# Optimization experiments

Hardware: AMD Instinct MI355X
Metric: run time of the kernel (lower is better)

The kernel has to match this reference:

```python
import jax, jax.numpy as jnp
import numpy as np

N = 50000      # nodes
E = 600000     # edges (avg degree 12)
D = 128        # input_dim == hidden_dim (required: same Linear reused across pool layers)
OUT = 64       # output_dim
NUM_POOL = 2   # num_pool_layers


def setup_inputs() -> dict:
    key = jax.random.key(0)
    ks = jax.random.split(key, 8)
    s = 1.0 / np.sqrt(D)  # fan-in style scaling keeps repeated scatter-adds stable
    x = jax.random.normal(ks[0], (N, D), dtype=jnp.float32)
    edge_index = jax.random.randint(ks[1], (2, E), 0, N, dtype=jnp.int64)
    W1 = jax.random.normal(ks[2], (D, D), dtype=jnp.float32) * s
    b1 = jnp.zeros((D,), dtype=jnp.float32)
    W2 = jax.random.normal(ks[3], (D, D), dtype=jnp.float32) * s
    b2 = jnp.zeros((D,), dtype=jnp.float32)
    Wout = jax.random.normal(ks[4], (D, OUT), dtype=jnp.float32) * s
    bout = jnp.zeros((OUT,), dtype=jnp.float32)
    return {"x": x, "edge_index": edge_index, "W1": W1, "b1": b1,
            "W2": W2, "b2": b2, "Wout": Wout, "bout": bout}


def _gauss_seidel_pool(x, W, b, src, dst, num_layers):
    # PyG MessagePassing(aggr='add'): out[i] = sum_{edges (j->i)} lin(x[j]).
    # Nodes with no incoming edges become zero (propagate replaces x entirely).
    for _ in range(num_layers):
        m = x @ W + b                      # [N, out] linear once per node (== lin(x_j) per edge)
        x = jax.ops.segment_sum(m[src], dst, num_segments=N)  # gather + scatter-add
    return x


def reference(x, edge_index, W1, b1, W2, b2, Wout, bout):
    src = edge_index[0]  # x_j source
    dst = edge_index[1]  # aggregation target i
    h = _gauss_seidel_pool(x, W1, b1, src, dst, NUM_POOL)
    h = jax.nn.relu(h)                     # dropout = identity (eval mode)
    h = _gauss_seidel_pool(h, W2, b2, src, dst, NUM_POOL)
    h = jax.nn.relu(h)
    return h @ Wout + bout                 # [N, OUT]
```

## Files before the change

kernel.cpp:

```cpp
#include <hip/hip_runtime.h>


static inline int ceil_div(int a, int b) { return (a + b - 1) / b; }

typedef __attribute__((ext_vector_type(8))) short bf16x8;
typedef __attribute__((ext_vector_type(4))) float f32x4;
typedef __attribute__((ext_vector_type(2))) float f32x2;

__device__ inline unsigned short f2bf(float f) {
    unsigned u = __float_as_uint(f);
    return (unsigned short)((u + 0x7fffu + ((u >> 16) & 1u)) >> 16);
}

__device__ inline unsigned char f2fp8(float f) {
    return (unsigned char)(__builtin_amdgcn_cvt_pk_fp8_f32(f, 0.f, 0u, false) & 0xffu);
}


__device__ void wprep_dev(const float* __restrict__ W, unsigned short* __restrict__ hi,
                          int total, int C, int g0, int G) {
    for (int t = g0; t < total; t += G) {
        int j = t & 7;
        int lane = (t >> 3) & 63;
        int f = t >> 9;
        int c = f & 3, ct = f >> 2;
        int k = c * 32 + (lane >> 4) * 8 + j;
        int col = ct * 16 + (lane & 15);
        hi[t] = f2bf(W[(size_t)k * C + col]);
    }
}

__global__ __launch_bounds__(256) void prep_kernel(const float* __restrict__ x,
                                                   const float* __restrict__ W1,
                                                   const float* __restrict__ W2,
                                                   const float* __restrict__ Wout,
                                                   unsigned char* __restrict__ xb,
                                                   unsigned short* __restrict__ W1hi,
                                                   unsigned short* __restrict__ W2hi,
                                                   unsigned short* __restrict__ Wohi,
                                                   int* __restrict__ cursor,
                                                   unsigned* __restrict__ stat,
                                                   int N, int nChunks) {
    int g0 = blockIdx.x * 256 + threadIdx.x;
    int G = gridDim.x * 256;
    for (int i = g0; i < N; i += G) cursor[i] = 0;
    for (int i = g0; i < nChunks; i += G) stat[i] = 0;

    int nq = N * 32;
    for (int i = g0; i < nq; i += G) {
        float4 v = ((const float4*)x)[i];
        unsigned w = __builtin_amdgcn_cvt_pk_fp8_f32(v.x, v.y, 0u, false);
        w = __builtin_amdgcn_cvt_pk_fp8_f32(v.z, v.w, w, true);
        ((unsigned*)xb)[i] = w;
    }

    wprep_dev(W1, W1hi, 128 * 128, 128, g0, G);
    wprep_dev(W2, W2hi, 128 * 128, 128, g0, G);
    wprep_dev(Wout, Wohi, 128 * 64, 64, g0, G);
}


__global__ __launch_bounds__(256) void hist_kernel(const int* __restrict__ dst,
                                                   int* __restrict__ deg, int E) {
    int e = blockIdx.x * 256 + threadIdx.x;
    if (e < E) atomicAdd(&deg[dst[e]], 1);
}

__global__ __launch_bounds__(256) void scan_fuse_kernel(const int* __restrict__ deg,
                                                        int* __restrict__ rp,
                                                        int* __restrict__ cursor,
                                                        unsigned* __restrict__ stat,
                                                        int N) {
    __shared__ int s[256];
    int c = blockIdx.x, tid = threadIdx.x;
    int i = c * 256 + tid;
    int v = (i < N) ? deg[i] : 0;
    s[tid] = v;
    __syncthreads();
    for (int off = 1; off < 256; off <<= 1) {
        int t = (tid >= off) ? s[tid - off] : 0;
        __syncthreads();
        s[tid] += t;
        __syncthreads();
    }
    int loc = s[tid] - v;
    int tot = s[255];
    __syncthreads();
    if (tid == 0) atomicExch(&stat[c], (unsigned)tot | 0x80000000u);

    unsigned mine = 0;
    if (tid < c) {
        unsigned u;
        do { u = atomicAdd(&stat[tid], 0u); } while (!(u & 0x80000000u));
        mine = u & 0x7fffffffu;
    }
    s[tid] = (int)mine;
    __syncthreads();
    for (int off = 128; off >= 1; off >>= 1) {
        if (tid < off) s[tid] += s[tid + off];
        __syncthreads();
    }
    int prefix = s[0];
    if (i <= N) {
        int val = loc + prefix;
        rp[i] = val;
        if (i < N) cursor[i] = val;
    }
}

__global__ __launch_bounds__(256) void fill_kernel(const int* __restrict__ src,
                                                   const int* __restrict__ dst,
                                                   int* __restrict__ cursor,
                                                   unsigned short* __restrict__ es, int E) {
    int e = blockIdx.x * 256 + threadIdx.x;
    if (e < E) {
        int p = atomicAdd(&cursor[dst[e]], 1);
        es[p] = (unsigned short)src[e];
    }
}


__device__ inline void acc_fp8(float* a, uint2 v) {
    f32x2 p;
    p = __builtin_amdgcn_cvt_pk_f32_fp8(v.x, false); a[0] += p[0]; a[1] += p[1];
    p = __builtin_amdgcn_cvt_pk_f32_fp8(v.x, true);  a[2] += p[0]; a[3] += p[1];
    p = __builtin_amdgcn_cvt_pk_f32_fp8(v.y, false); a[4] += p[0]; a[5] += p[1];
    p = __builtin_amdgcn_cvt_pk_f32_fp8(v.y, true);  a[6] += p[0]; a[7] += p[1];
}

template <bool RELU, bool OUTCHAIN>
__global__ __launch_bounds__(256) void fused_kernel(const unsigned char* __restrict__ M,
                                                    const int* __restrict__ rp,
                                                    const unsigned short* __restrict__ es,
                                                    const uint4* __restrict__ Whi,
                                                    const float* __restrict__ bvec,
                                                    const uint4* __restrict__ Wof,
                                                    const float* __restrict__ bout,
                                                    void* __restrict__ Yv, int n) {
    constexpr int SR = 136;
    constexpr int ECAP = 1280;
    __shared__ unsigned short Hl[64 * SR];
    __shared__ unsigned short esl[ECAP];
    __shared__ int rpl[65];
    __shared__ unsigned char perm[64];

    int tid = threadIdx.x;
    int r0 = blockIdx.x * 64;

    if (tid < 65) {
        int gi = r0 + tid;
        if (gi > n) gi = n;
        rpl[tid] = rp[gi];
    }
    __syncthreads();

    int ebase = rpl[0];
    int ecnt = rpl[64] - ebase;
    if (ecnt > ECAP) ecnt = ECAP;

    if (tid < 64) {
        int di = rpl[tid + 1] - rpl[tid];
        int rank = 0;
        for (int j = 0; j < 64; ++j) {
            int dj = rpl[j + 1] - rpl[j];
            rank += (dj > di) || (dj == di && j < tid);
        }
        perm[rank] = (unsigned char)tid;
    }
    for (int i = tid; i < ecnt; i += 256) esl[i] = es[ebase + i];
    __syncthreads();

    {
        int g = tid >> 4, ln = tid & 15;
        const unsigned char* Mh = M + ln * 8;
#pragma unroll 1
        for (int q = 0; q < 4; ++q) {
            int nl = perm[q * 16 + g];
            int pbeg = rpl[nl] - ebase, pend = rpl[nl + 1] - ebase;
            int pm = pend < ecnt ? pend : ecnt;
            float acc[8] = {};
            int p = pbeg;
            for (; p + 8 <= pm; p += 8) {
                int s0 = esl[p],     s1 = esl[p + 1], s2 = esl[p + 2], s3 = esl[p + 3];
                int s4 = esl[p + 4], s5 = esl[p + 5], s6 = esl[p + 6], s7 = esl[p + 7];
                uint2 v0 = *(const uint2*)(Mh + (size_t)s0 * 128);
                uint2 v1 = *(const uint2*)(Mh + (size_t)s1 * 128);
                uint2 v2 = *(const uint2*)(Mh + (size_t)s2 * 128);
                uint2 v3 = *(const uint2*)(Mh + (size_t)s3 * 128);
                uint2 v4 = *(const uint2*)(Mh + (size_t)s4 * 128);
                uint2 v5 = *(const uint2*)(Mh + (size_t)s5 * 128);
                uint2 v6 = *(const uint2*)(Mh + (size_t)s6 * 128);
                uint2 v7 = *(const uint2*)(Mh + (size_t)s7 * 128);
                acc_fp8(acc, v0); acc_fp8(acc, v1);
                acc_fp8(acc, v2); acc_fp8(acc, v3);
                acc_fp8(acc, v4); acc_fp8(acc, v5);
                acc_fp8(acc, v6); acc_fp8(acc, v7);
            }
            for (; p + 4 <= pm; p += 4) {
                int s0 = esl[p], s1 = esl[p + 1], s2 = esl[p + 2], s3 = esl[p + 3];
                uint2 v0 = *(const uint2*)(Mh + (size_t)s0 * 128);
                uint2 v1 = *(const uint2*)(Mh + (size_t)s1 * 128);
                uint2 v2 = *(const uint2*)(Mh + (size_t)s2 * 128);
                uint2 v3 = *(const uint2*)(Mh + (size_t)s3 * 128);
                acc_fp8(acc, v0); acc_fp8(acc, v1);
                acc_fp8(acc, v2); acc_fp8(acc, v3);
            }
            for (; p < pm; ++p) {
                uint2 v = *(const uint2*)(Mh + (size_t)esl[p] * 128);
                acc_fp8(acc, v);
            }
            for (; p < pend; ++p) {
                uint2 v = *(const uint2*)(Mh + (size_t)es[ebase + p] * 128);
                acc_fp8(acc, v);
            }
            uint4 o;
            o.x = (unsigned)f2bf(acc[0]) | ((unsigned)f2bf(acc[1]) << 16);
            o.y = (unsigned)f2bf(acc[2]) | ((unsigned)f2bf(acc[3]) << 16);
            o.z = (unsigned)f2bf(acc[4]) | ((unsigned)f2bf(acc[5]) << 16);
            o.w = (unsigned)f2bf(acc[6]) | ((unsigned)f2bf(acc[7]) << 16);
            *(uint4*)(&Hl[nl * SR + ln * 8]) = o;
        }
    }
    __syncthreads();

    int wave = tid >> 6, lane = tid & 63;
    int lm = lane & 15, lq = lane >> 4;

    f32x4 acc[4][2];
#pragma unroll
    for (int rt = 0; rt < 4; ++rt)
#pragma unroll
        for (int t = 0; t < 2; ++t)
            acc[rt][t] = (f32x4){0.f, 0.f, 0.f, 0.f};

#pragma unroll
    for (int c = 0; c < 4; ++c) {
        bf16x8 afr[4];
#pragma unroll
        for (int rt = 0; rt < 4; ++rt)
            afr[rt] = *(const bf16x8*)(&Hl[(rt * 16 + lm) * SR + c * 32 + lq * 8]);
#pragma unroll
        for (int t = 0; t < 2; ++t) {
            int ct = wave * 2 + t;
            uint4 uh = Whi[(ct * 4 + c) * 64 + lane];
            bf16x8 wh = *(const bf16x8*)&uh;
#pragma unroll
            for (int rt = 0; rt < 4; ++rt)
                acc[rt][t] = __builtin_amdgcn_mfma_f32_16x16x32_bf16(afr[rt], wh, acc[rt][t], 0, 0, 0);
        }
    }

    if (!OUTCHAIN) {
#pragma unroll
        for (int t = 0; t < 2; ++t) {
            int col = (wave * 2 + t) * 16 + lm;
            float bv = bvec[col];
#pragma unroll
            for (int rt = 0; rt < 4; ++rt) {
#pragma unroll
                for (int r = 0; r < 4; ++r) {
                    int rowl = rt * 16 + lq * 4 + r;
                    int row = r0 + rowl;
                    if (row < n) {
                        float deg = (float)(rpl[rowl + 1] - rpl[rowl]);
                        float v = acc[rt][t][r] + deg * bv;
                        if (RELU) v = fmaxf(v, 0.f);
                        ((unsigned char*)Yv)[(size_t)row * 128 + col] = f2fp8(v);
                    }
                }
            }
        }
    } else {
        __syncthreads();
#pragma unroll
        for (int t = 0; t < 2; ++t) {
            int col = (wave * 2 + t) * 16 + lm;
            float bv = bvec[col];
#pragma unroll
            for (int rt = 0; rt < 4; ++rt) {
#pragma unroll
                for (int r = 0; r < 4; ++r) {
                    int rowl = rt * 16 + lq * 4 + r;
                    float deg = (float)(rpl[rowl + 1] - rpl[rowl]);
                    float v = acc[rt][t][r] + deg * bv;
                    v = fmaxf(v, 0.f);
                    Hl[rowl * SR + col] = f2bf(v);
                }
            }
        }
        __syncthreads();

        f32x4 acc2[4];
#pragma unroll
        for (int rt = 0; rt < 4; ++rt) acc2[rt] = (f32x4){0.f, 0.f, 0.f, 0.f};

#pragma unroll
        for (int c = 0; c < 4; ++c) {
            bf16x8 afr[4];
#pragma unroll
            for (int rt = 0; rt < 4; ++rt)
                afr[rt] = *(const bf16x8*)(&Hl[(rt * 16 + lm) * SR + c * 32 + lq * 8]);
            uint4 uw = Wof[(wave * 4 + c) * 64 + lane];
            bf16x8 wf = *(const bf16x8*)&uw;
#pragma unroll
            for (int rt = 0; rt < 4; ++rt)
                acc2[rt] = __builtin_amdgcn_mfma_f32_16x16x32_bf16(afr[rt], wf, acc2[rt], 0, 0, 0);
        }

        int col = wave * 16 + lm;
        float bo = bout[col];
#pragma unroll
        for (int rt = 0; rt < 4; ++rt) {
#pragma unroll
            for (int r = 0; r < 4; ++r) {
                int row = r0 + rt * 16 + lq * 4 + r;
                if (row < n)
                    ((float*)Yv)[(size_t)row * 64 + col] = acc2[rt][r] + bo;
            }
        }
    }
}


extern "C" void kernel_launch(void* const* d_in, const int* in_sizes, int n_in,
                              void* d_out, int out_size, void* d_ws, size_t ws_size,
                              hipStream_t stream) {
    const float* x    = (const float*)d_in[0];
    const int*   ei   = (const int*)d_in[1];
    const float* W1   = (const float*)d_in[2];
    const float* b1   = (const float*)d_in[3];
    const float* W2   = (const float*)d_in[4];
    const float* b2   = (const float*)d_in[5];
    const float* Wout = (const float*)d_in[6];
    const float* bout = (const float*)d_in[7];
    float*       out  = (float*)d_out;

    const int N = in_sizes[0] / 128;
    const int E = in_sizes[1] / 2;
    const int* src = ei;
    const int* dst = ei + E;

    char* ws = (char*)d_ws;
    auto take = [&](size_t bytes) {
        char* p = ws;
        ws += (bytes + 255) & ~(size_t)255;
        return p;
    };
    unsigned char* xb = (unsigned char*)take((size_t)N * 128);
    unsigned char* mA = (unsigned char*)take((size_t)N * 128);
    unsigned char* mB = (unsigned char*)take((size_t)N * 128);
    unsigned short* W1hi = (unsigned short*)take(128 * 128 * 2);
    unsigned short* W2hi = (unsigned short*)take(128 * 128 * 2);
    unsigned short* Wohi = (unsigned short*)take(128 * 64 * 2);
    int* rp      = (int*)take((size_t)(N + 1) * sizeof(int));
    int* cursor  = (int*)take((size_t)N * sizeof(int));
    unsigned short* es = (unsigned short*)take((size_t)E * sizeof(unsigned short));
    unsigned* stat = (unsigned*)take(4096);

    const int nChunks = ceil_div(N + 1, 256);
    const int tiles64 = ceil_div(N, 64);

    prep_kernel<<<256, 256, 0, stream>>>(x, W1, W2, Wout, xb, W1hi, W2hi, Wohi,
                                         cursor, stat, N, nChunks);
    hist_kernel<<<ceil_div(E, 256), 256, 0, stream>>>(dst, cursor, E);
    scan_fuse_kernel<<<nChunks, 256, 0, stream>>>(cursor, rp, cursor, stat, N);
    fill_kernel<<<ceil_div(E, 256), 256, 0, stream>>>(src, dst, cursor, es, E);

    fused_kernel<false, false><<<tiles64, 256, 0, stream>>>(
        xb, rp, es, (const uint4*)W1hi, b1, nullptr, nullptr, mA, N);
    fused_kernel<true, false><<<tiles64, 256, 0, stream>>>(
        mA, rp, es, (const uint4*)W1hi, b1, nullptr, nullptr, mB, N);
    fused_kernel<false, false><<<tiles64, 256, 0, stream>>>(
        mB, rp, es, (const uint4*)W2hi, b2, nullptr, nullptr, mA, N);
    fused_kernel<true, true><<<tiles64, 256, 0, stream>>>(
        mA, rp, es, (const uint4*)W2hi, b2, (const uint4*)Wohi, bout, out, N);
}
```

Measured before the change: 254.8 us.

## Split fused gather+GEMM into separate passes over column-slab fp8 layout

Stores fp8 node features as two 64-column slabs so each gather block touches a smaller, more cache-resident working set, and splits each layer into a gather pass (two blocks per tile, one per slab, 16-byte loads) and a separate MFMA GEMM pass that reads the aggregated bf16 rows from a global buffer. The gather also warms L2 for its slab with a prefetch load. This trades an extra bf16 round trip through global memory and four extra launches for better gather locality and parallelism.

```diff
diff --git a/kernel.cpp b/kernel.cpp
--- a/kernel.cpp
+++ b/kernel.cpp
@@ -34,7 +34,7 @@
                                                    const float* __restrict__ W1,
                                                    const float* __restrict__ W2,
                                                    const float* __restrict__ Wout,
-                                                   unsigned char* __restrict__ xb,
+                                                   unsigned* __restrict__ xb,
                                                    unsigned short* __restrict__ W1hi,
                                                    unsigned short* __restrict__ W2hi,
                                                    unsigned short* __restrict__ Wohi,
@@ -51,7 +51,9 @@
         float4 v = ((const float4*)x)[i];
         unsigned w = __builtin_amdgcn_cvt_pk_fp8_f32(v.x, v.y, 0u, false);
         w = __builtin_amdgcn_cvt_pk_fp8_f32(v.z, v.w, w, true);
-        ((unsigned*)xb)[i] = w;
+        int row = i >> 5, j = i & 31;
+        int s = j >> 4;
+        xb[(size_t)s * N * 16 + (size_t)row * 16 + (j & 15)] = w;
     }
 
     wprep_dev(W1, W1hi, 128 * 128, 128, g0, G);
@@ -120,32 +122,43 @@
 }
 
 
-__device__ inline void acc_fp8(float* a, uint2 v) {
+__device__ inline void acc16f(float* a, uint4 v) {
     f32x2 p;
-    p = __builtin_amdgcn_cvt_pk_f32_fp8(v.x, false); a[0] += p[0]; a[1] += p[1];
-    p = __builtin_amdgcn_cvt_pk_f32_fp8(v.x, true);  a[2] += p[0]; a[3] += p[1];
-    p = __builtin_amdgcn_cvt_pk_f32_fp8(v.y, false); a[4] += p[0]; a[5] += p[1];
-    p = __builtin_amdgcn_cvt_pk_f32_fp8(v.y, true);  a[6] += p[0]; a[7] += p[1];
-}
-
-template <bool RELU, bool OUTCHAIN>
-__global__ __launch_bounds__(256) void fused_kernel(const unsigned char* __restrict__ M,
-                                                    const int* __restrict__ rp,
-                                                    const unsigned short* __restrict__ es,
-                                                    const uint4* __restrict__ Whi,
-                                                    const float* __restrict__ bvec,
-                                                    const uint4* __restrict__ Wof,
-                                                    const float* __restrict__ bout,
-                                                    void* __restrict__ Yv, int n) {
-    constexpr int SR = 136;
+    p = __builtin_amdgcn_cvt_pk_f32_fp8(v.x, false); a[0] += p[0];  a[1] += p[1];
+    p = __builtin_amdgcn_cvt_pk_f32_fp8(v.x, true);  a[2] += p[0];  a[3] += p[1];
+    p = __builtin_amdgcn_cvt_pk_f32_fp8(v.y, false); a[4] += p[0];  a[5] += p[1];
+    p = __builtin_amdgcn_cvt_pk_f32_fp8(v.y, true);  a[6] += p[0];  a[7] += p[1];
+    p = __builtin_amdgcn_cvt_pk_f32_fp8(v.z, false); a[8] += p[0];  a[9] += p[1];
+    p = __builtin_amdgcn_cvt_pk_f32_fp8(v.z, true);  a[10] += p[0]; a[11] += p[1];
+    p = __builtin_amdgcn_cvt_pk_f32_fp8(v.w, false); a[12] += p[0]; a[13] += p[1];
+    p = __builtin_amdgcn_cvt_pk_f32_fp8(v.w, true);  a[14] += p[0]; a[15] += p[1];
+}
+
+__global__ __launch_bounds__(256) void gather_pass(const unsigned char* __restrict__ Ms,
+                                                   const int* __restrict__ rp,
+                                                   const unsigned short* __restrict__ es,
+                                                   unsigned short* __restrict__ H,
+                                                   int n, int N) {
     constexpr int ECAP = 1280;
-    __shared__ unsigned short Hl[64 * SR];
     __shared__ unsigned short esl[ECAP];
     __shared__ int rpl[65];
     __shared__ unsigned char perm[64];
 
     int tid = threadIdx.x;
-    int r0 = blockIdx.x * 64;
+    int s = blockIdx.x & 1;
+    int t = blockIdx.x >> 1;
+    int r0 = t * 64;
+
+    const unsigned char* slab = Ms + (size_t)s * N * 64;
+
+    {
+        size_t off = ((size_t)(t >> 2) * 256 + tid) * 64;
+        if (off + 64 <= (size_t)N * 64) {
+            const uint4* wp = (const uint4*)(slab + off);
+            uint4 a0 = wp[0], a1 = wp[1], a2 = wp[2], a3 = wp[3];
+            asm volatile("" :: "v"(a0.x), "v"(a1.y), "v"(a2.z), "v"(a3.w));
+        }
+    }
 
     if (tid < 65) {
         int gi = r0 + tid;
@@ -170,56 +183,80 @@
     for (int i = tid; i < ecnt; i += 256) esl[i] = es[ebase + i];
     __syncthreads();
 
-    {
-        int g = tid >> 4, ln = tid & 15;
-        const unsigned char* Mh = M + ln * 8;
-#pragma unroll 1
-        for (int q = 0; q < 4; ++q) {
-            int nl = perm[q * 16 + g];
-            int pbeg = rpl[nl] - ebase, pend = rpl[nl + 1] - ebase;
-            int pm = pend < ecnt ? pend : ecnt;
-            float acc[8] = {};
-            int p = pbeg;
-            for (; p + 8 <= pm; p += 8) {
-                int s0 = esl[p],     s1 = esl[p + 1], s2 = esl[p + 2], s3 = esl[p + 3];
-                int s4 = esl[p + 4], s5 = esl[p + 5], s6 = esl[p + 6], s7 = esl[p + 7];
-                uint2 v0 = *(const uint2*)(Mh + (size_t)s0 * 128);
-                uint2 v1 = *(const uint2*)(Mh + (size_t)s1 * 128);
-                uint2 v2 = *(const uint2*)(Mh + (size_t)s2 * 128);
-                uint2 v3 = *(const uint2*)(Mh + (size_t)s3 * 128);
-                uint2 v4 = *(const uint2*)(Mh + (size_t)s4 * 128);
-                uint2 v5 = *(const uint2*)(Mh + (size_t)s5 * 128);
-                uint2 v6 = *(const uint2*)(Mh + (size_t)s6 * 128);
-                uint2 v7 = *(const uint2*)(Mh + (size_t)s7 * 128);
-                acc_fp8(acc, v0); acc_fp8(acc, v1);
-                acc_fp8(acc, v2); acc_fp8(acc, v3);
-                acc_fp8(acc, v4); acc_fp8(acc, v5);
-                acc_fp8(acc, v6); acc_fp8(acc, v7);
-            }
-            for (; p + 4 <= pm; p += 4) {
-                int s0 = esl[p], s1 = esl[p + 1], s2 = esl[p + 2], s3 = esl[p + 3];
-                uint2 v0 = *(const uint2*)(Mh + (size_t)s0 * 128);
-                uint2 v1 = *(const uint2*)(Mh + (size_t)s1 * 128);
-                uint2 v2 = *(const uint2*)(Mh + (size_t)s2 * 128);
-                uint2 v3 = *(const uint2*)(Mh + (size_t)s3 * 128);
-                acc_fp8(acc, v0); acc_fp8(acc, v1);
-                acc_fp8(acc, v2); acc_fp8(acc, v3);
-            }
-            for (; p < pm; ++p) {
-                uint2 v = *(const uint2*)(Mh + (size_t)esl[p] * 128);
-                acc_fp8(acc, v);
-            }
-            for (; p < pend; ++p) {
-                uint2 v = *(const uint2*)(Mh + (size_t)es[ebase + p] * 128);
-                acc_fp8(acc, v);
-            }
-            uint4 o;
-            o.x = (unsigned)f2bf(acc[0]) | ((unsigned)f2bf(acc[1]) << 16);
-            o.y = (unsigned)f2bf(acc[2]) | ((unsigned)f2bf(acc[3]) << 16);
-            o.z = (unsigned)f2bf(acc[4]) | ((unsigned)f2bf(acc[5]) << 16);
-            o.w = (unsigned)f2bf(acc[6]) | ((unsigned)f2bf(acc[7]) << 16);
-            *(uint4*)(&Hl[nl * SR + ln * 8]) = o;
-        }
+    int gid = tid >> 2, ln = tid & 3;
+    int nl = perm[gid];
+    int beg = rpl[nl], end = rpl[nl + 1];
+    int pbeg = beg - ebase, pend = end - ebase;
+    int pm = pend < ecnt ? pend : ecnt;
+    const unsigned char* base = slab + ln * 16;
+
+    float a[16] = {};
+    int p = pbeg;
+    for (; p + 8 <= pm; p += 8) {
+        int s0 = esl[p],     s1 = esl[p + 1], s2 = esl[p + 2], s3 = esl[p + 3];
+        int s4 = esl[p + 4], s5 = esl[p + 5], s6 = esl[p + 6], s7 = esl[p + 7];
+        uint4 v0 = *(const uint4*)(base + (size_t)s0 * 64);
+        uint4 v1 = *(const uint4*)(base + (size_t)s1 * 64);
+        uint4 v2 = *(const uint4*)(base + (size_t)s2 * 64);
+        uint4 v3 = *(const uint4*)(base + (size_t)s3 * 64);
+        uint4 v4 = *(const uint4*)(base + (size_t)s4 * 64);
+        uint4 v5 = *(const uint4*)(base + (size_t)s5 * 64);
+        uint4 v6 = *(const uint4*)(base + (size_t)s6 * 64);
+        uint4 v7 = *(const uint4*)(base + (size_t)s7 * 64);
+        acc16f(a, v0); acc16f(a, v1); acc16f(a, v2); acc16f(a, v3);
+        acc16f(a, v4); acc16f(a, v5); acc16f(a, v6); acc16f(a, v7);
+    }
+    for (; p + 4 <= pm; p += 4) {
+        int s0 = esl[p], s1 = esl[p + 1], s2 = esl[p + 2], s3 = esl[p + 3];
+        uint4 v0 = *(const uint4*)(base + (size_t)s0 * 64);
+        uint4 v1 = *(const uint4*)(base + (size_t)s1 * 64);
+        uint4 v2 = *(const uint4*)(base + (size_t)s2 * 64);
+        uint4 v3 = *(const uint4*)(base + (size_t)s3 * 64);
+        acc16f(a, v0); acc16f(a, v1); acc16f(a, v2); acc16f(a, v3);
+    }
+    for (; p < pm; ++p) {
+        uint4 v = *(const uint4*)(base + (size_t)esl[p] * 64);
+        acc16f(a, v);
+    }
+    for (; p < pend; ++p) {
+        uint4 v = *(const uint4*)(base + (size_t)es[ebase + p] * 64);
+        acc16f(a, v);
+    }
+
+    int node = r0 + nl;
+    if (node < n) {
+        unsigned long long* dst =
+            (unsigned long long*)(H + (size_t)node * 128 + s * 64 + ln * 16);
+#pragma unroll
+        for (int k = 0; k < 4; ++k) {
+            unsigned lo = (unsigned)f2bf(a[4 * k + 0]) | ((unsigned)f2bf(a[4 * k + 1]) << 16);
+            unsigned hi = (unsigned)f2bf(a[4 * k + 2]) | ((unsigned)f2bf(a[4 * k + 3]) << 16);
+            unsigned long long o = (unsigned long long)lo | ((unsigned long long)hi << 32);
+            __builtin_nontemporal_store(o, dst + k);
+        }
+    }
+}
+
+
+template <bool RELU, bool OUTCHAIN>
+__global__ __launch_bounds__(256) void gemm_pass(const unsigned short* __restrict__ H,
+                                                 const uint4* __restrict__ Whi,
+                                                 const float* __restrict__ bvec,
+                                                 const int* __restrict__ rp,
+                                                 const uint4* __restrict__ Wof,
+                                                 const float* __restrict__ bout,
+                                                 void* __restrict__ Yv, int n, int N) {
+    constexpr int SR = 136;
+    __shared__ unsigned short Hl[64 * SR];
+    __shared__ int rpl[65];
+
+    int tid = threadIdx.x;
+    int r0 = blockIdx.x * 64;
+
+    if (tid < 65) {
+        int gi = r0 + tid;
+        if (gi > n) gi = n;
+        rpl[tid] = rp[gi];
     }
     __syncthreads();
 
@@ -238,11 +275,10 @@
         bf16x8 afr[4];
 #pragma unroll
         for (int rt = 0; rt < 4; ++rt)
-            afr[rt] = *(const bf16x8*)(&Hl[(rt * 16 + lm) * SR + c * 32 + lq * 8]);
+            afr[rt] = *(const bf16x8*)(H + (size_t)(r0 + rt * 16 + lm) * 128 + c * 32 + lq * 8);
 #pragma unroll
         for (int t = 0; t < 2; ++t) {
-            int ct = wave * 2 + t;
-            uint4 uh = Whi[(ct * 4 + c) * 64 + lane];
+            uint4 uh = Whi[((wave * 2 + t) * 4 + c) * 64 + lane];
             bf16x8 wh = *(const bf16x8*)&uh;
 #pragma unroll
             for (int rt = 0; rt < 4; ++rt)
@@ -254,6 +290,7 @@
 #pragma unroll
         for (int t = 0; t < 2; ++t) {
             int col = (wave * 2 + t) * 16 + lm;
+            int sl = col >> 6, c64 = col & 63;
             float bv = bvec[col];
 #pragma unroll
             for (int rt = 0; rt < 4; ++rt) {
@@ -265,13 +302,12 @@
                         float deg = (float)(rpl[rowl + 1] - rpl[rowl]);
                         float v = acc[rt][t][r] + deg * bv;
                         if (RELU) v = fmaxf(v, 0.f);
-                        ((unsigned char*)Yv)[(size_t)row * 128 + col] = f2fp8(v);
+                        ((unsigned char*)Yv)[(size_t)sl * N * 64 + (size_t)row * 64 + c64] = f2fp8(v);
                     }
                 }
             }
         }
     } else {
-        __syncthreads();
 #pragma unroll
         for (int t = 0; t < 2; ++t) {
             int col = (wave * 2 + t) * 16 + lm;
@@ -340,15 +376,18 @@
     const int* src = ei;
     const int* dst = ei + E;
 
+    const int tiles64 = ceil_div(N, 64);
+    const int nChunks = ceil_div(N + 1, 256);
+
     char* ws = (char*)d_ws;
     auto take = [&](size_t bytes) {
         char* p = ws;
         ws += (bytes + 255) & ~(size_t)255;
         return p;
     };
-    unsigned char* xb = (unsigned char*)take((size_t)N * 128);
-    unsigned char* mA = (unsigned char*)take((size_t)N * 128);
-    unsigned char* mB = (unsigned char*)take((size_t)N * 128);
+    unsigned char* mS0 = (unsigned char*)take((size_t)N * 128);
+    unsigned char* mS1 = (unsigned char*)take((size_t)N * 128);
+    unsigned short* Hb = (unsigned short*)take((size_t)tiles64 * 64 * 128 * 2);
     unsigned short* W1hi = (unsigned short*)take(128 * 128 * 2);
     unsigned short* W2hi = (unsigned short*)take(128 * 128 * 2);
     unsigned short* Wohi = (unsigned short*)take(128 * 64 * 2);
@@ -357,21 +396,22 @@
     unsigned short* es = (unsigned short*)take((size_t)E * sizeof(unsigned short));
     unsigned* stat = (unsigned*)take(4096);
 
-    const int nChunks = ceil_div(N + 1, 256);
-    const int tiles64 = ceil_div(N, 64);
-
-    prep_kernel<<<256, 256, 0, stream>>>(x, W1, W2, Wout, xb, W1hi, W2hi, Wohi,
-                                         cursor, stat, N, nChunks);
+    prep_kernel<<<256, 256, 0, stream>>>(x, W1, W2, Wout, (unsigned*)mS0,
+                                         W1hi, W2hi, Wohi, cursor, stat, N, nChunks);
     hist_kernel<<<ceil_div(E, 256), 256, 0, stream>>>(dst, cursor, E);
     scan_fuse_kernel<<<nChunks, 256, 0, stream>>>(cursor, rp, cursor, stat, N);
     fill_kernel<<<ceil_div(E, 256), 256, 0, stream>>>(src, dst, cursor, es, E);
 
-    fused_kernel<false, false><<<tiles64, 256, 0, stream>>>(
-        xb, rp, es, (const uint4*)W1hi, b1, nullptr, nullptr, mA, N);
-    fused_kernel<true, false><<<tiles64, 256, 0, stream>>>(
-        mA, rp, es, (const uint4*)W1hi, b1, nullptr, nullptr, mB, N);
-    fused_kernel<false, false><<<tiles64, 256, 0, stream>>>(
-        mB, rp, es, (const uint4*)W2hi, b2, nullptr, nullptr, mA, N);
-    fused_kernel<true, true><<<tiles64, 256, 0, stream>>>(
-        mA, rp, es, (const uint4*)W2hi, b2, (const uint4*)Wohi, bout, out, N);
-}
+    gather_pass<<<tiles64 * 2, 256, 0, stream>>>(mS0, rp, es, Hb, N, N);
+    gemm_pass<false, false><<<tiles64, 256, 0, stream>>>(Hb, (const uint4*)W1hi, b1, rp,
+                                                         nullptr, nullptr, mS1, N, N);
+    gather_pass<<<tiles64 * 2, 256, 0, stream>>>(mS1, rp, es, Hb, N, N);
+    gemm_pass<true, false><<<tiles64, 256, 0, stream>>>(Hb, (const uint4*)W1hi, b1, rp,
+                                                        nullptr, nullptr, mS0, N, N);
+    gather_pass<<<tiles64 * 2, 256, 0, stream>>>(mS0, rp, es, Hb, N, N);
+    gemm_pass<false, false><<<tiles64, 256, 0, stream>>>(Hb, (const uint4*)W2hi, b2, rp,
+                                                         nullptr, nullptr, mS1, N, N);
+    gather_pass<<<tiles64 * 2, 256, 0, stream>>>(mS1, rp, es, Hb, N, N);
+    gemm_pass<true, true><<<tiles64, 256, 0, stream>>>(Hb, (const uint4*)W2hi, b2, rp,
+                                                       (const uint4*)Wohi, bout, out, N, N);
+}
```

Result: slower. 297.2 us (+16.7%).

## Fuse CSR build into one grid-synced kernel and widen gather loads to 16 bytes

Applied to the files above, without the earlier changes.

Merges the histogram, scan and fill kernels into a single persistent csr_kernel that uses atomic grid barriers between phases, removing two kernel launches and their gaps. The gather phase of the fused kernel now has each thread load 16 fp8 features (uint4) instead of 8. Each of 32 node groups handles two nodes paired from opposite ends of the degree ranking, to balance work. The grid barrier relies on all ~196 blocks being co-resident, which would deadlock if they are not. The wider loads cut the number of threads per node, which may lower memory-level parallelism.

```diff
diff --git a/kernel.cpp b/kernel.cpp
--- a/kernel.cpp
+++ b/kernel.cpp
@@ -40,11 +40,11 @@
                                                    unsigned short* __restrict__ Wohi,
                                                    int* __restrict__ cursor,
                                                    unsigned* __restrict__ stat,
-                                                   int N, int nChunks) {
+                                                   int N) {
     int g0 = blockIdx.x * 256 + threadIdx.x;
     int G = gridDim.x * 256;
     for (int i = g0; i < N; i += G) cursor[i] = 0;
-    for (int i = g0; i < nChunks; i += G) stat[i] = 0;
+    for (int i = g0; i < 1024; i += G) stat[i] = 0;
 
     int nq = N * 32;
     for (int i = g0; i < nq; i += G) {
@@ -60,21 +60,33 @@
 }
 
 
-__global__ __launch_bounds__(256) void hist_kernel(const int* __restrict__ dst,
-                                                   int* __restrict__ deg, int E) {
-    int e = blockIdx.x * 256 + threadIdx.x;
-    if (e < E) atomicAdd(&deg[dst[e]], 1);
-}
-
-__global__ __launch_bounds__(256) void scan_fuse_kernel(const int* __restrict__ deg,
-                                                        int* __restrict__ rp,
-                                                        int* __restrict__ cursor,
-                                                        unsigned* __restrict__ stat,
-                                                        int N) {
+__device__ inline void grid_barrier(unsigned* ctr, unsigned target) {
+    __syncthreads();
+    __threadfence();
+    if (threadIdx.x == 0) {
+        atomicAdd(ctr, 1u);
+        while (atomicAdd(ctr, 0u) < target) {}
+    }
+    __syncthreads();
+}
+
+__global__ __launch_bounds__(256) void csr_kernel(const int* __restrict__ src,
+                                                  const int* __restrict__ dst,
+                                                  int* __restrict__ rp,
+                                                  int* __restrict__ cursor,
+                                                  unsigned short* __restrict__ es,
+                                                  unsigned* __restrict__ stat,
+                                                  int N, int E) {
     __shared__ int s[256];
     int c = blockIdx.x, tid = threadIdx.x;
+    int g0 = c * 256 + tid, G = gridDim.x * 256;
+
+    for (int e = g0; e < E; e += G) atomicAdd(&cursor[dst[e]], 1);
+
+    grid_barrier(&stat[512], gridDim.x);
+
     int i = c * 256 + tid;
-    int v = (i < N) ? deg[i] : 0;
+    int v = (i < N) ? atomicAdd(&cursor[i], 0) : 0;
     s[tid] = v;
     __syncthreads();
     for (int off = 1; off < 256; off <<= 1) {
@@ -104,28 +116,28 @@
     if (i <= N) {
         int val = loc + prefix;
         rp[i] = val;
-        if (i < N) cursor[i] = val;
-    }
-}
-
-__global__ __launch_bounds__(256) void fill_kernel(const int* __restrict__ src,
-                                                   const int* __restrict__ dst,
-                                                   int* __restrict__ cursor,
-                                                   unsigned short* __restrict__ es, int E) {
-    int e = blockIdx.x * 256 + threadIdx.x;
-    if (e < E) {
+        if (i < N) atomicExch(&cursor[i], val);
+    }
+
+    grid_barrier(&stat[513], gridDim.x);
+
+    for (int e = g0; e < E; e += G) {
         int p = atomicAdd(&cursor[dst[e]], 1);
         es[p] = (unsigned short)src[e];
     }
 }
 
 
-__device__ inline void acc_fp8(float* a, uint2 v) {
+__device__ inline void acc16f(float* a, uint4 v) {
     f32x2 p;
-    p = __builtin_amdgcn_cvt_pk_f32_fp8(v.x, false); a[0] += p[0]; a[1] += p[1];
-    p = __builtin_amdgcn_cvt_pk_f32_fp8(v.x, true);  a[2] += p[0]; a[3] += p[1];
-    p = __builtin_amdgcn_cvt_pk_f32_fp8(v.y, false); a[4] += p[0]; a[5] += p[1];
-    p = __builtin_amdgcn_cvt_pk_f32_fp8(v.y, true);  a[6] += p[0]; a[7] += p[1];
+    p = __builtin_amdgcn_cvt_pk_f32_fp8(v.x, false); a[0] += p[0];  a[1] += p[1];
+    p = __builtin_amdgcn_cvt_pk_f32_fp8(v.x, true);  a[2] += p[0];  a[3] += p[1];
+    p = __builtin_amdgcn_cvt_pk_f32_fp8(v.y, false); a[4] += p[0];  a[5] += p[1];
+    p = __builtin_amdgcn_cvt_pk_f32_fp8(v.y, true);  a[6] += p[0];  a[7] += p[1];
+    p = __builtin_amdgcn_cvt_pk_f32_fp8(v.z, false); a[8] += p[0];  a[9] += p[1];
+    p = __builtin_amdgcn_cvt_pk_f32_fp8(v.z, true);  a[10] += p[0]; a[11] += p[1];
+    p = __builtin_amdgcn_cvt_pk_f32_fp8(v.w, false); a[12] += p[0]; a[13] += p[1];
+    p = __builtin_amdgcn_cvt_pk_f32_fp8(v.w, true);  a[14] += p[0]; a[15] += p[1];
 }
 
 template <bool RELU, bool OUTCHAIN>
@@ -171,54 +183,43 @@
     __syncthreads();
 
     {
-        int g = tid >> 4, ln = tid & 15;
-        const unsigned char* Mh = M + ln * 8;
+        int g = tid >> 3, ln = tid & 7;
+        const unsigned char* Mh = M + ln * 16;
 #pragma unroll 1
-        for (int q = 0; q < 4; ++q) {
-            int nl = perm[q * 16 + g];
+        for (int q = 0; q < 2; ++q) {
+            int nl = perm[q ? (63 - g) : g];
             int pbeg = rpl[nl] - ebase, pend = rpl[nl + 1] - ebase;
             int pm = pend < ecnt ? pend : ecnt;
-            float acc[8] = {};
+            float acc[16] = {};
             int p = pbeg;
-            for (; p + 8 <= pm; p += 8) {
-                int s0 = esl[p],     s1 = esl[p + 1], s2 = esl[p + 2], s3 = esl[p + 3];
-                int s4 = esl[p + 4], s5 = esl[p + 5], s6 = esl[p + 6], s7 = esl[p + 7];
-                uint2 v0 = *(const uint2*)(Mh + (size_t)s0 * 128);
-                uint2 v1 = *(const uint2*)(Mh + (size_t)s1 * 128);
-                uint2 v2 = *(const uint2*)(Mh + (size_t)s2 * 128);
-                uint2 v3 = *(const uint2*)(Mh + (size_t)s3 * 128);
-                uint2 v4 = *(const uint2*)(Mh + (size_t)s4 * 128);
-                uint2 v5 = *(const uint2*)(Mh + (size_t)s5 * 128);
-                uint2 v6 = *(const uint2*)(Mh + (size_t)s6 * 128);
-                uint2 v7 = *(const uint2*)(Mh + (size_t)s7 * 128);
-                acc_fp8(acc, v0); acc_fp8(acc, v1);
-                acc_fp8(acc, v2); acc_fp8(acc, v3);
-                acc_fp8(acc, v4); acc_fp8(acc, v5);
-                acc_fp8(acc, v6); acc_fp8(acc, v7);
-            }
             for (; p + 4 <= pm; p += 4) {
                 int s0 = esl[p], s1 = esl[p + 1], s2 = esl[p + 2], s3 = esl[p + 3];
-                uint2 v0 = *(const uint2*)(Mh + (size_t)s0 * 128);
-                uint2 v1 = *(const uint2*)(Mh + (size_t)s1 * 128);
-                uint2 v2 = *(const uint2*)(Mh + (size_t)s2 * 128);
-                uint2 v3 = *(const uint2*)(Mh + (size_t)s3 * 128);
-                acc_fp8(acc, v0); acc_fp8(acc, v1);
-                acc_fp8(acc, v2); acc_fp8(acc, v3);
+                uint4 v0 = *(const uint4*)(Mh + (size_t)s0 * 128);
+                uint4 v1 = *(const uint4*)(Mh + (size_t)s1 * 128);
+                uint4 v2 = *(const uint4*)(Mh + (size_t)s2 * 128);
+                uint4 v3 = *(const uint4*)(Mh + (size_t)s3 * 128);
+                acc16f(acc, v0); acc16f(acc, v1);
+                acc16f(acc, v2); acc16f(acc, v3);
             }
             for (; p < pm; ++p) {
-                uint2 v = *(const uint2*)(Mh + (size_t)esl[p] * 128);
-                acc_fp8(acc, v);
+                uint4 v = *(const uint4*)(Mh + (size_t)esl[p] * 128);
+                acc16f(acc, v);
             }
             for (; p < pend; ++p) {
-                uint2 v = *(const uint2*)(Mh + (size_t)es[ebase + p] * 128);
-                acc_fp8(acc, v);
-            }
-            uint4 o;
-            o.x = (unsigned)f2bf(acc[0]) | ((unsigned)f2bf(acc[1]) << 16);
-            o.y = (unsigned)f2bf(acc[2]) | ((unsigned)f2bf(acc[3]) << 16);
-            o.z = (unsigned)f2bf(acc[4]) | ((unsigned)f2bf(acc[5]) << 16);
-            o.w = (unsigned)f2bf(acc[6]) | ((unsigned)f2bf(acc[7]) << 16);
-            *(uint4*)(&Hl[nl * SR + ln * 8]) = o;
+                uint4 v = *(const uint4*)(Mh + (size_t)es[ebase + p] * 128);
+                acc16f(acc, v);
+            }
+            uint4 o0, o1;
+            o0.x = (unsigned)f2bf(acc[0])  | ((unsigned)f2bf(acc[1])  << 16);
+            o0.y = (unsigned)f2bf(acc[2])  | ((unsigned)f2bf(acc[3])  << 16);
+            o0.z = (unsigned)f2bf(acc[4])  | ((unsigned)f2bf(acc[5])  << 16);
+            o0.w = (unsigned)f2bf(acc[6])  | ((unsigned)f2bf(acc[7])  << 16);
+            o1.x = (unsigned)f2bf(acc[8])  | ((unsigned)f2bf(acc[9])  << 16);
+            o1.y = (unsigned)f2bf(acc[10]) | ((unsigned)f2bf(acc[11]) << 16);
+            o1.z = (unsigned)f2bf(acc[12]) | ((unsigned)f2bf(acc[13]) << 16);
+            o1.w = (unsigned)f2bf(acc[14]) | ((unsigned)f2bf(acc[15]) << 16);
+            *(uint4*)(&Hl[nl * SR + ln * 16]) = o0;
+            *(uint4*)(&Hl[nl * SR + ln * 16 + 8]) = o1;
         }
     }
     __syncthreads();
@@ -361,10 +362,8 @@
     const int tiles64 = ceil_div(N, 64);
 
     prep_kernel<<<256, 256, 0, stream>>>(x, W1, W2, Wout, xb, W1hi, W2hi, Wohi,
-                                         cursor, stat, N, nChunks);
-    hist_kernel<<<ceil_div(E, 256), 256, 0, stream>>>(dst, cursor, E);
-    scan_fuse_kernel<<<nChunks, 256, 0, stream>>>(cursor, rp, cursor, stat, N);
-    fill_kernel<<<ceil_div(E, 256), 256, 0, stream>>>(src, dst, cursor, es, E);
+                                         cursor, stat, N);
+    csr_kernel<<<nChunks, 256, 0, stream>>>(src, dst, rp, cursor, es, stat, N, E);
 
     fused_kernel<false, false><<<tiles64, 256, 0, stream>>>(
         xb, rp, es, (const uint4*)W1hi, b1, nullptr, nullptr, mA, N);
```

Result: slower. 314.1 us (+23.3%).
